# Kernel tuning notes

Measured on AMD Instinct MI355X. Metric: run time of the kernel, lower is better.

## Reference

```python
import jax, jax.numpy as jnp
import numpy as np

FEATURES = 4
HIDDEN = 32


def setup_inputs() -> dict:
    key = jax.random.key(0)
    ks = jax.random.split(key, 12)
    n_nodes, n_edges = 100000, 2500000
    x = jax.random.normal(ks[0], (n_nodes, FEATURES), dtype=jnp.float32)
    edge_index = jax.random.randint(ks[1], (2, n_edges), 0, n_nodes, dtype=jnp.int64)
    def glorot(k, fan_in, fan_out):
        s = jnp.sqrt(6.0 / (fan_in + fan_out)).astype(jnp.float32)
        return jax.random.uniform(k, (fan_in, fan_out), jnp.float32, -s, s)
    return {
        "x": x,
        "edge_index": edge_index,
        "W1": glorot(ks[2], FEATURES, HIDDEN), "b1": jnp.zeros((HIDDEN,), jnp.float32),
        "W2": glorot(ks[3], HIDDEN, HIDDEN),   "b2": jnp.zeros((HIDDEN,), jnp.float32),
        "W21": glorot(ks[4], HIDDEN, HIDDEN),  "b21": jnp.zeros((HIDDEN,), jnp.float32),
        "W3": glorot(ks[5], HIDDEN, 1),        "b3": jnp.zeros((1,), jnp.float32),
    }


def _gcn_norm(edge_index, n_nodes):
    # Add self-loops, compute symmetric normalization deg^-1/2[dst]*deg^-1/2[src]
    loops = jnp.arange(n_nodes, dtype=edge_index.dtype)
    src = jnp.concatenate([edge_index[0], loops])
    dst = jnp.concatenate([edge_index[1], loops])
    deg = jax.ops.segment_sum(jnp.ones_like(dst, dtype=jnp.float32), dst, num_segments=n_nodes)
    dinv = jnp.where(deg > 0, jax.lax.rsqrt(deg), 0.0)
    norm = dinv[src] * dinv[dst]  # [E+N]
    return src, dst, norm


def _gcn_layer(x, W, b, src, dst, norm, n_nodes):
    h = x @ W                                   # [N, out]
    msg = h[src] * norm[:, None]                # gather + scale
    out = jax.ops.segment_sum(msg, dst, num_segments=n_nodes)  # scatter-add
    return out + b


def reference(x, edge_index, W1, b1, W2, b2, W21, b21, W3, b3):
    n_nodes = x.shape[0]
    src, dst, norm = _gcn_norm(edge_index, n_nodes)
    h = jax.nn.relu(_gcn_layer(x, W1, b1, src, dst, norm, n_nodes))
    h = jax.nn.relu(_gcn_layer(h, W2, b2, src, dst, norm, n_nodes))
    h = jax.nn.relu(_gcn_layer(h, W21, b21, src, dst, norm, n_nodes))
    return _gcn_layer(h, W3, b3, src, dst, norm, n_nodes)
```

## Files before the change

kernel.cpp:

```cpp
#include <hip/hip_runtime.h>

#define FEATS 4
#define HID 32
#define BLK 256
#define CAP 64
#define PW 256
#define PSHIFT 8
#define PCAP 8192
#define NPB 512
#define PBLK 1024
#define MAXK 8
#define MAXNP 512

static inline int cdiv(long long a, int b) { return (int)((a + b - 1) / b); }

__global__ void k_zero_i(int* __restrict__ p, int n) {
    int i = blockIdx.x * blockDim.x + threadIdx.x;
    if (i < n) p[i] = 0;
}

__global__ void __launch_bounds__(PBLK, 4)
k_partition(const int* __restrict__ src, const int* __restrict__ dst,
            int* __restrict__ part_fill, unsigned int* __restrict__ part_edges,
            int e, int np) {
    __shared__ int lcnt[MAXNP];
    __shared__ int lbase[MAXNP];
    for (int p = threadIdx.x; p < np; p += blockDim.x) lcnt[p] = 0;
    __syncthreads();
    int chunk = (e + gridDim.x - 1) / gridDim.x;
    int lo = blockIdx.x * chunk;
    int hi = min(lo + chunk, e);
    unsigned pw[MAXK];
    int pp[MAXK];
#pragma unroll
    for (int k = 0; k < MAXK; k++) {
        int j = lo + threadIdx.x + k * (int)blockDim.x;
        if (j < hi) {
            int d = dst[j], s = src[j];
            int p = d >> PSHIFT;
            pp[k] = p;
            pw[k] = (unsigned)s | ((unsigned)(d & (PW - 1)) << 24);
            atomicAdd(&lcnt[p], 1);
        } else pp[k] = -1;
    }
    __syncthreads();
    for (int p = threadIdx.x; p < np; p += blockDim.x) {
        int c = lcnt[p];
        lbase[p] = c ? atomicAdd(&part_fill[p], c) : 0;
        lcnt[p] = 0;
    }
    __syncthreads();
#pragma unroll
    for (int k = 0; k < MAXK; k++) {
        if (pp[k] >= 0) {
            int p = pp[k];
            int pos = lbase[p] + atomicAdd(&lcnt[p], 1);
            if (pos < PCAP) part_edges[(size_t)p * PCAP + pos] = pw[k];
        }
    }
}

__global__ void k_local_csr(const int* __restrict__ part_fill,
                            const unsigned int* __restrict__ part_edges,
                            const float4* __restrict__ x,
                            int* __restrict__ cnt_g, float* __restrict__ dinv,
                            float4* __restrict__ xn, int* __restrict__ bucket, int n) {
    __shared__ int cnt[PW];
    int p = blockIdx.x;
    if (threadIdx.x < PW) cnt[threadIdx.x] = 0;
    __syncthreads();
    int m = min(part_fill[p], PCAP);
    const unsigned int* pe = part_edges + (size_t)p * PCAP;
    int base_node = p << PSHIFT;
    for (int j = threadIdx.x; j < m; j += blockDim.x) {
        unsigned v = pe[j];
        int local = (int)(v >> 24);
        int s = (int)(v & 0xFFFFFFu);
        int pos = atomicAdd(&cnt[local], 1);
        if (pos < CAP) bucket[(size_t)(base_node + local) * CAP + pos] = s;
    }
    __syncthreads();
    if (threadIdx.x < PW) {
        int node = base_node + threadIdx.x;
        if (node < n) {
            int dg = cnt[threadIdx.x];
            cnt_g[node] = dg;
            float s = rsqrtf((float)(dg + 1));
            dinv[node] = s;
            float4 v = x[node];
            v.x *= s; v.y *= s; v.z *= s; v.w *= s;
            xn[node] = v;
        }
    }
}

__global__ void k_dinv(const int* __restrict__ deg, float* __restrict__ dinv, int n) {
    int i = blockIdx.x * blockDim.x + threadIdx.x;
    if (i < n) dinv[i] = rsqrtf((float)(deg[i] + 1));
}

__global__ void k_gather4_f12(const int* __restrict__ cnt, const int* __restrict__ bucket,
                              const float4* __restrict__ xn, const float* __restrict__ dinv,
                              const float* __restrict__ W1, const float* __restrict__ b1,
                              const float* __restrict__ W2, float* __restrict__ hn, int n) {
    __shared__ float4 sW1[FEATS * 8];
    __shared__ float4 sB1[8];
    __shared__ float4 sW2[HID * 8];
    int tid = threadIdx.x;
    if (tid < FEATS * 8) sW1[tid] = ((const float4*)W1)[tid];
    if (tid < 8) sB1[tid] = ((const float4*)b1)[tid];
    sW2[tid] = ((const float4*)W2)[tid];
    __syncthreads();
    int gid = blockIdx.x * blockDim.x + tid;
    int node = gid >> 3;
    int cq = gid & 7;
    if (node >= n) return;
    int dg = min(cnt[node], CAP);
    const int* row = bucket + (size_t)node * CAP;
    float4 acc = make_float4(0.f, 0.f, 0.f, 0.f);
    int j = cq;
    for (; j + 8 < dg; j += 16) {
        int s0 = row[j], s1 = row[j + 8];
        float4 v0 = xn[s0];
        float4 v1 = xn[s1];
        acc.x += v0.x + v1.x; acc.y += v0.y + v1.y;
        acc.z += v0.z + v1.z; acc.w += v0.w + v1.w;
    }
    if (j < dg) {
        float4 v = xn[row[j]];
        acc.x += v.x; acc.y += v.y; acc.z += v.z; acc.w += v.w;
    }
#pragma unroll
    for (int m = 1; m < 8; m <<= 1) {
        acc.x += __shfl_xor(acc.x, m, 8);
        acc.y += __shfl_xor(acc.y, m, 8);
        acc.z += __shfl_xor(acc.z, m, 8);
        acc.w += __shfl_xor(acc.w, m, 8);
    }
    float sc = dinv[node];
    float4 self = xn[node];
    float4 a;
    a.x = sc * (acc.x + self.x);
    a.y = sc * (acc.y + self.y);
    a.z = sc * (acc.z + self.z);
    a.w = sc * (acc.w + self.w);
    float4 w0 = sW1[0 * 8 + cq], w1 = sW1[1 * 8 + cq];
    float4 w2 = sW1[2 * 8 + cq], w3 = sW1[3 * 8 + cq];
    float4 y = sB1[cq];
    y.x += a.x * w0.x + a.y * w1.x + a.z * w2.x + a.w * w3.x;
    y.y += a.x * w0.y + a.y * w1.y + a.z * w2.y + a.w * w3.y;
    y.z += a.x * w0.z + a.y * w1.z + a.z * w2.z + a.w * w3.z;
    y.w += a.x * w0.w + a.y * w1.w + a.z * w2.w + a.w * w3.w;
    y.x = fmaxf(y.x, 0.f); y.y = fmaxf(y.y, 0.f);
    y.z = fmaxf(y.z, 0.f); y.w = fmaxf(y.w, 0.f);
    float4 o = make_float4(0.f, 0.f, 0.f, 0.f);
#pragma unroll
    for (int r = 0; r < 8; r++) {
        float4 v;
        v.x = __shfl(y.x, r, 8);
        v.y = __shfl(y.y, r, 8);
        v.z = __shfl(y.z, r, 8);
        v.w = __shfl(y.w, r, 8);
        float4 wa = sW2[(4 * r + 0) * 8 + cq];
        float4 wb = sW2[(4 * r + 1) * 8 + cq];
        float4 wc = sW2[(4 * r + 2) * 8 + cq];
        float4 wd = sW2[(4 * r + 3) * 8 + cq];
        o.x += v.x * wa.x + v.y * wb.x + v.z * wc.x + v.w * wd.x;
        o.y += v.x * wa.y + v.y * wb.y + v.z * wc.y + v.w * wd.y;
        o.z += v.x * wa.z + v.y * wb.z + v.z * wc.z + v.w * wd.z;
        o.w += v.x * wa.w + v.y * wb.w + v.z * wc.w + v.w * wd.w;
    }
    o.x *= sc; o.y *= sc; o.z *= sc; o.w *= sc;
    ((float4*)hn)[node * 8 + cq] = o;
}

template <int K, int C>
__global__ void k_mm(const float* __restrict__ in, const float* __restrict__ W,
                     const float* __restrict__ dinv, float* __restrict__ hn, int n) {
    __shared__ float sW[K * C];
    for (int i = threadIdx.x; i < K * C; i += blockDim.x) sW[i] = W[i];
    __syncthreads();
    int gid = blockIdx.x * blockDim.x + threadIdx.x;
    int node = gid / C, c = gid % C;
    if (node >= n) return;
    float acc = 0.0f;
#pragma unroll
    for (int k = 0; k < K; k++) acc += in[node * K + k] * sW[k * C + c];
    hn[node * C + c] = acc * dinv[node];
}

#define ACC4(v) do { acc.x += (v).x; acc.y += (v).y; acc.z += (v).z; acc.w += (v).w; } while (0)

#define GATHER_BODY()                                                        \
    int dg = min(cnt[node], CAP);                                            \
    const float4* hp = (const float4*)hn;                                    \
    const int* row = bucket + (size_t)node * CAP;                            \
    float4 acc = hp[node * 8 + cq];                                          \
    int j = 0;                                                               \
    for (; j + 8 <= dg; j += 8) {                                            \
        int4 sa = *(const int4*)(row + j);                                   \
        int4 sb = *(const int4*)(row + j + 4);                               \
        float4 v0 = hp[sa.x * 8 + cq];                                       \
        float4 v1 = hp[sa.y * 8 + cq];                                       \
        float4 v2 = hp[sa.z * 8 + cq];                                       \
        float4 v3 = hp[sa.w * 8 + cq];                                       \
        float4 v4 = hp[sb.x * 8 + cq];                                       \
        float4 v5 = hp[sb.y * 8 + cq];                                       \
        float4 v6 = hp[sb.z * 8 + cq];                                       \
        float4 v7 = hp[sb.w * 8 + cq];                                       \
        ACC4(v0); ACC4(v1); ACC4(v2); ACC4(v3);                              \
        ACC4(v4); ACC4(v5); ACC4(v6); ACC4(v7);                              \
    }                                                                        \
    if (j + 4 <= dg) {                                                       \
        int4 s4 = *(const int4*)(row + j);                                   \
        float4 v0 = hp[s4.x * 8 + cq];                                       \
        float4 v1 = hp[s4.y * 8 + cq];                                       \
        float4 v2 = hp[s4.z * 8 + cq];                                       \
        float4 v3 = hp[s4.w * 8 + cq];                                       \
        ACC4(v0); ACC4(v1); ACC4(v2); ACC4(v3);                              \
        j += 4;                                                              \
    }                                                                        \
    for (; j < dg; j++) {                                                    \
        float4 v = hp[row[j] * 8 + cq];                                      \
        ACC4(v);                                                             \
    }

__global__ void k_gather_fmm(const int* __restrict__ cnt, const int* __restrict__ bucket,
                             const float* __restrict__ hn, const float* __restrict__ dinv,
                             const float* __restrict__ bias, const float* __restrict__ Wn,
                             float* __restrict__ hn3, int n) {
    __shared__ float4 sW[HID * 8];
    sW[threadIdx.x] = ((const float4*)Wn)[threadIdx.x];
    __syncthreads();
    int gid = blockIdx.x * blockDim.x + threadIdx.x;
    int node = gid >> 3;
    int cq = gid & 7;
    if (node >= n) return;
    GATHER_BODY()
    float sc = dinv[node];
    float4 b = ((const float4*)bias)[cq];
    float4 y;
    y.x = fmaxf(sc * acc.x + b.x, 0.f);
    y.y = fmaxf(sc * acc.y + b.y, 0.f);
    y.z = fmaxf(sc * acc.z + b.z, 0.f);
    y.w = fmaxf(sc * acc.w + b.w, 0.f);
    float4 o = make_float4(0.f, 0.f, 0.f, 0.f);
#pragma unroll
    for (int r = 0; r < 8; r++) {
        float4 v;
        v.x = __shfl(y.x, r, 8);
        v.y = __shfl(y.y, r, 8);
        v.z = __shfl(y.z, r, 8);
        v.w = __shfl(y.w, r, 8);
        float4 w0 = sW[(4 * r + 0) * 8 + cq];
        float4 w1 = sW[(4 * r + 1) * 8 + cq];
        float4 w2 = sW[(4 * r + 2) * 8 + cq];
        float4 w3 = sW[(4 * r + 3) * 8 + cq];
        o.x += v.x * w0.x + v.y * w1.x + v.z * w2.x + v.w * w3.x;
        o.y += v.x * w0.y + v.y * w1.y + v.z * w2.y + v.w * w3.y;
        o.z += v.x * w0.z + v.y * w1.z + v.z * w2.z + v.w * w3.z;
        o.w += v.x * w0.w + v.y * w1.w + v.z * w2.w + v.w * w3.w;
    }
    o.x *= sc; o.y *= sc; o.z *= sc; o.w *= sc;
    ((float4*)hn3)[node * 8 + cq] = o;
}

__global__ void k_gather_fdot(const int* __restrict__ cnt, const int* __restrict__ bucket,
                              const float* __restrict__ hn, const float* __restrict__ dinv,
                              const float* __restrict__ bias, const float* __restrict__ W3,
                              float* __restrict__ hn4, int n) {
    int gid = blockIdx.x * blockDim.x + threadIdx.x;
    int node = gid >> 3;
    int cq = gid & 7;
    if (node >= n) return;
    GATHER_BODY()
    float sc = dinv[node];
    float4 b = ((const float4*)bias)[cq];
    float4 w = ((const float4*)W3)[cq];
    float p = fmaxf(sc * acc.x + b.x, 0.f) * w.x
            + fmaxf(sc * acc.y + b.y, 0.f) * w.y
            + fmaxf(sc * acc.z + b.z, 0.f) * w.z
            + fmaxf(sc * acc.w + b.w, 0.f) * w.w;
#pragma unroll
    for (int o = 4; o > 0; o >>= 1) p += __shfl_down(p, o, 8);
    if (cq == 0) hn4[node] = p * sc;
}

__global__ void k_gather1b(const int* __restrict__ cnt, const int* __restrict__ bucket,
                           const float* __restrict__ hn, const float* __restrict__ dinv,
                           const float* __restrict__ b, float* __restrict__ out, int n) {
    int gid = blockIdx.x * blockDim.x + threadIdx.x;
    int node = gid >> 3;
    int lane = gid & 7;
    if (node >= n) return;
    int dg = min(cnt[node], CAP);
    const int* row = bucket + (size_t)node * CAP;
    float acc = (lane == 0) ? hn[node] : 0.0f;
    int j = lane;
    for (; j + 8 < dg; j += 16) {
        float a0 = hn[row[j]];
        float a1 = hn[row[j + 8]];
        acc += a0 + a1;
    }
    if (j < dg) acc += hn[row[j]];
#pragma unroll
    for (int o = 4; o > 0; o >>= 1) acc += __shfl_down(acc, o, 8);
    if (lane == 0) out[node] = dinv[node] * acc + b[0];
}

__global__ void k_deg_count(const int* __restrict__ dst, int* __restrict__ deg, int e) {
    int i = blockIdx.x * blockDim.x + threadIdx.x;
    if (i < e) atomicAdd(&deg[dst[i]], 1);
}

__global__ void k_block_scan(const int* __restrict__ deg, int* __restrict__ exc,
                             int* __restrict__ blk_sums, int n) {
    __shared__ int s[BLK];
    int i = blockIdx.x * BLK + threadIdx.x;
    int v = (i < n) ? deg[i] : 0;
    s[threadIdx.x] = v;
    __syncthreads();
    for (int off = 1; off < BLK; off <<= 1) {
        int t = (threadIdx.x >= (unsigned)off) ? s[threadIdx.x - off] : 0;
        __syncthreads();
        s[threadIdx.x] += t;
        __syncthreads();
    }
    if (i < n) exc[i] = s[threadIdx.x] - v;
    if (threadIdx.x == BLK - 1) blk_sums[blockIdx.x] = s[threadIdx.x];
}

__global__ void k_scan_sums(int* __restrict__ blk_sums, int nb) {
    __shared__ int s[1024];
    __shared__ int carry;
    if (threadIdx.x == 0) carry = 0;
    __syncthreads();
    for (int base = 0; base < nb; base += 1024) {
        int i = base + threadIdx.x;
        int v = (i < nb) ? blk_sums[i] : 0;
        s[threadIdx.x] = v;
        __syncthreads();
        for (int off = 1; off < 1024; off <<= 1) {
            int t = (threadIdx.x >= (unsigned)off) ? s[threadIdx.x - off] : 0;
            __syncthreads();
            s[threadIdx.x] += t;
            __syncthreads();
        }
        if (i < nb) blk_sums[i] = s[threadIdx.x] - v + carry;
        __syncthreads();
        if (threadIdx.x == 0) carry += s[1023];
        __syncthreads();
    }
}

__global__ void k_add_off(const int* __restrict__ exc, const int* __restrict__ blk_sums,
                          int* __restrict__ row_start, int* __restrict__ fill, int n) {
    int i = blockIdx.x * blockDim.x + threadIdx.x;
    if (i < n) {
        int rs = exc[i] + blk_sums[i / BLK];
        row_start[i] = rs;
        fill[i] = rs;
    }
}

__global__ void k_scatter(const int* __restrict__ src, const int* __restrict__ dst,
                          int* __restrict__ fill, int* __restrict__ csr_src, int e) {
    int i = blockIdx.x * blockDim.x + threadIdx.x;
    if (i < e) {
        int pos = atomicAdd(&fill[dst[i]], 1);
        csr_src[pos] = src[i];
    }
}

template <bool RELU>
__global__ void k_gather32(const int* __restrict__ row_start, const int* __restrict__ deg,
                           const int* __restrict__ csr_src, const float* __restrict__ hn,
                           const float* __restrict__ dinv, const float* __restrict__ bias,
                           float* __restrict__ y, int n) {
    int gid = blockIdx.x * blockDim.x + threadIdx.x;
    int node = gid >> 3;
    int cq = gid & 7;
    if (node >= n) return;
    int rs = row_start[node], dg = deg[node];
    const float4* hp = (const float4*)hn;
    float4 acc = hp[node * 8 + cq];
    for (int j = 0; j < dg; j++) {
        int s = csr_src[rs + j];
        float4 v = hp[s * 8 + cq];
        ACC4(v);
    }
    float sc = dinv[node];
    float4 b = ((const float4*)bias)[cq];
    float4 r;
    r.x = sc * acc.x + b.x; r.y = sc * acc.y + b.y;
    r.z = sc * acc.z + b.z; r.w = sc * acc.w + b.w;
    if (RELU) {
        r.x = fmaxf(r.x, 0.0f); r.y = fmaxf(r.y, 0.0f);
        r.z = fmaxf(r.z, 0.0f); r.w = fmaxf(r.w, 0.0f);
    }
    ((float4*)y)[node * 8 + cq] = r;
}

__global__ void k_gather1(const int* __restrict__ row_start, const int* __restrict__ deg,
                          const int* __restrict__ csr_src, const float* __restrict__ hn,
                          const float* __restrict__ dinv, const float* __restrict__ b,
                          float* __restrict__ out, int n) {
    int gid = blockIdx.x * blockDim.x + threadIdx.x;
    int node = gid >> 3;
    int lane = gid & 7;
    if (node >= n) return;
    int rs = row_start[node], dg = deg[node];
    float acc = (lane == 0) ? hn[node] : 0.0f;
    for (int j = lane; j < dg; j += 8) acc += hn[csr_src[rs + j]];
#pragma unroll
    for (int o = 4; o > 0; o >>= 1) acc += __shfl_down(acc, o, 8);
    if (lane == 0) out[node] = dinv[node] * acc + b[0];
}

extern "C" void kernel_launch(void* const* d_in, const int* in_sizes, int n_in,
                              void* d_out, int out_size, void* d_ws, size_t ws_size,
                              hipStream_t stream) {
    const float* x   = (const float*)d_in[0];
    const int*   ei  = (const int*)d_in[1];
    const float* W1  = (const float*)d_in[2];
    const float* b1  = (const float*)d_in[3];
    const float* W2  = (const float*)d_in[4];
    const float* b2  = (const float*)d_in[5];
    const float* W21 = (const float*)d_in[6];
    const float* b21 = (const float*)d_in[7];
    const float* W3  = (const float*)d_in[8];
    const float* b3  = (const float*)d_in[9];
    float* out = (float*)d_out;

    const int n = in_sizes[0] / FEATS;
    const int e = in_sizes[1] / 2;
    const int* src = ei;
    const int* dst = ei + e;
    const int nb = cdiv(n, BLK);
    const int np = cdiv(n, PW);

    auto align256 = [](size_t v) { return (v + 255) & ~(size_t)255; };
    const long long n8 = (long long)n * 8;

    size_t sz_cnt    = align256((size_t)n * 4);
    size_t sz_dinv   = align256((size_t)n * 4);
    size_t sz_f4     = align256((size_t)n * 16);
    size_t sz_bucket = align256((size_t)n * CAP * 4);
    size_t sz_hn     = align256((size_t)n * HID * 4);
    size_t sz_part   = align256((size_t)np * PCAP * 4) + align256((size_t)np * 4);
    size_t region    = 2 * sz_hn > sz_part ? 2 * sz_hn : sz_part;
    size_t need = sz_cnt + sz_dinv + sz_f4 + sz_bucket + region;

    if (ws_size >= need && np <= MAXNP && (long long)e <= (long long)NPB * PBLK * MAXK) {
        char* ws = (char*)d_ws;
        size_t off = 0;
        int*    cnt_g  = (int*)(ws + off);    off += sz_cnt;
        float*  dinv   = (float*)(ws + off);  off += sz_dinv;
        float4* xn     = (float4*)(ws + off); off += sz_f4;
        int*    bucket = (int*)(ws + off);    off += sz_bucket;
        char*   reg    = ws + off;
        float* hn = (float*)reg;
        float* yb = (float*)(reg + sz_hn);
        unsigned int* part_edges = (unsigned int*)reg;
        int* part_fill = (int*)(reg + align256((size_t)np * PCAP * 4));

        k_zero_i<<<cdiv(np, BLK), BLK, 0, stream>>>(part_fill, np);
        k_partition<<<NPB, PBLK, 0, stream>>>(src, dst, part_fill, part_edges, e, np);
        k_local_csr<<<np, PBLK, 0, stream>>>(part_fill, part_edges, (const float4*)x,
                                             cnt_g, dinv, xn, bucket, n);

        k_gather4_f12<<<cdiv(n8, BLK), BLK, 0, stream>>>(cnt_g, bucket, xn, dinv,
                                                         W1, b1, W2, hn, n);

        k_gather_fmm<<<cdiv(n8, BLK), BLK, 0, stream>>>(cnt_g, bucket, hn, dinv, b2, W21, yb, n);
        k_gather_fdot<<<cdiv(n8, BLK), BLK, 0, stream>>>(cnt_g, bucket, yb, dinv, b21, W3, hn, n);
        k_gather1b<<<cdiv(n8, BLK), BLK, 0, stream>>>(cnt_g, bucket, hn, dinv, b3, out, n);
    } else {
        const long long nc = (long long)n * HID;
        char* ws = (char*)d_ws;
        size_t off = 0;
        int*   deg_i     = (int*)(ws + off);   off += align256((size_t)n * 4);
        int*   exc       = (int*)(ws + off);   off += align256((size_t)n * 4);
        int*   row_start = (int*)(ws + off);   off += align256((size_t)n * 4);
        int*   fill      = (int*)(ws + off);   off += align256((size_t)n * 4);
        int*   blk_sums  = (int*)(ws + off);   off += align256((size_t)nb * 4);
        float* dinv      = (float*)(ws + off); off += align256((size_t)n * 4);
        int*   csr_src   = (int*)(ws + off);   off += align256((size_t)e * 4);
        float* hn        = (float*)(ws + off); off += align256((size_t)n * HID * 4);
        float* yb        = (float*)(ws + off); off += align256((size_t)n * HID * 4);

        k_zero_i<<<nb, BLK, 0, stream>>>(deg_i, n);
        k_deg_count<<<cdiv(e, BLK), BLK, 0, stream>>>(dst, deg_i, e);
        k_dinv<<<nb, BLK, 0, stream>>>(deg_i, dinv, n);
        k_block_scan<<<nb, BLK, 0, stream>>>(deg_i, exc, blk_sums, n);
        k_scan_sums<<<1, 1024, 0, stream>>>(blk_sums, nb);
        k_add_off<<<nb, BLK, 0, stream>>>(exc, blk_sums, row_start, fill, n);
        k_scatter<<<cdiv(e, BLK), BLK, 0, stream>>>(src, dst, fill, csr_src, e);

        k_mm<FEATS, HID><<<cdiv(nc, BLK), BLK, 0, stream>>>(x, W1, dinv, hn, n);
        k_gather32<true><<<cdiv(n8, BLK), BLK, 0, stream>>>(row_start, deg_i, csr_src, hn, dinv, b1, yb, n);

        k_mm<HID, HID><<<cdiv(nc, BLK), BLK, 0, stream>>>(yb, W2, dinv, hn, n);
        k_gather32<true><<<cdiv(n8, BLK), BLK, 0, stream>>>(row_start, deg_i, csr_src, hn, dinv, b2, yb, n);

        k_mm<HID, HID><<<cdiv(nc, BLK), BLK, 0, stream>>>(yb, W21, dinv, hn, n);
        k_gather32<true><<<cdiv(n8, BLK), BLK, 0, stream>>>(row_start, deg_i, csr_src, hn, dinv, b21, yb, n);

        k_mm<HID, 1><<<cdiv(n, BLK), BLK, 0, stream>>>(yb, W3, dinv, hn, n);
        k_gather1<<<cdiv(n8, BLK), BLK, 0, stream>>>(row_start, deg_i, csr_src, hn, dinv, b3, out, n);
    }
}
```

Baseline: 243.7 us.

## Replace global-atomic partitioning with per-block fixed-size runs plus overflow buffer

The partition kernel no longer reserves space with a global atomic per partition and a second shared-memory pass. Each block now writes its edges straight into a fixed slot of 32 entries per (partition, block) pair, and only the rare excess goes through a global overflow buffer. The local CSR kernel then scans every block's run for its partition, using the per-block counts. This removes the two-phase reservation and most global atomics. In exchange the CSR kernel scans sparse runs that are largely empty, and edges beyond the overflow capacity of 64 per partition would be silently dropped.

```diff
diff --git a/kernel.cpp b/kernel.cpp
--- a/kernel.cpp
+++ b/kernel.cpp
@@ -6,11 +6,12 @@
 #define CAP 64
 #define PW 256
 #define PSHIFT 8
-#define PCAP 8192
 #define NPB 512
 #define PBLK 1024
-#define MAXK 8
 #define MAXNP 512
+#define RCAP 32
+#define RSHIFT 5
+#define OCAP 64
 
 static inline int cdiv(long long a, int b) { return (int)((a + b - 1) / b); }
 
@@ -19,65 +20,69 @@
     if (i < n) p[i] = 0;
 }
 
-__global__ void __launch_bounds__(PBLK, 4)
-k_partition(const int* __restrict__ src, const int* __restrict__ dst,
-            int* __restrict__ part_fill, unsigned int* __restrict__ part_edges,
-            int e, int np) {
+__global__ void __launch_bounds__(PBLK, 2)
+k_part_s(const int* __restrict__ src, const int* __restrict__ dst,
+         unsigned int* __restrict__ runs, int* __restrict__ cnt_runs,
+         int* __restrict__ ovf_fill, unsigned int* __restrict__ ovf,
+         int e, int np) {
     __shared__ int lcnt[MAXNP];
-    __shared__ int lbase[MAXNP];
     for (int p = threadIdx.x; p < np; p += blockDim.x) lcnt[p] = 0;
     __syncthreads();
     int chunk = (e + gridDim.x - 1) / gridDim.x;
     int lo = blockIdx.x * chunk;
     int hi = min(lo + chunk, e);
-    unsigned pw[MAXK];
-    int pp[MAXK];
-#pragma unroll
-    for (int k = 0; k < MAXK; k++) {
-        int j = lo + threadIdx.x + k * (int)blockDim.x;
-        if (j < hi) {
-            int d = dst[j], s = src[j];
-            int p = d >> PSHIFT;
-            pp[k] = p;
-            pw[k] = (unsigned)s | ((unsigned)(d & (PW - 1)) << 24);
-            atomicAdd(&lcnt[p], 1);
-        } else pp[k] = -1;
-    }
-    __syncthreads();
-    for (int p = threadIdx.x; p < np; p += blockDim.x) {
-        int c = lcnt[p];
-        lbase[p] = c ? atomicAdd(&part_fill[p], c) : 0;
-        lcnt[p] = 0;
-    }
-    __syncthreads();
-#pragma unroll
-    for (int k = 0; k < MAXK; k++) {
-        if (pp[k] >= 0) {
-            int p = pp[k];
-            int pos = lbase[p] + atomicAdd(&lcnt[p], 1);
-            if (pos < PCAP) part_edges[(size_t)p * PCAP + pos] = pw[k];
+    for (int j = lo + threadIdx.x; j < hi; j += blockDim.x) {
+        int d = dst[j], s = src[j];
+        int p = d >> PSHIFT;
+        unsigned pk = (unsigned)s | ((unsigned)(d & (PW - 1)) << 24);
+        int pos = atomicAdd(&lcnt[p], 1);
+        if (pos < RCAP) {
+            runs[((size_t)p * NPB + blockIdx.x) * RCAP + pos] = pk;
+        } else {
+            int q = atomicAdd(&ovf_fill[p], 1);
+            if (q < OCAP) ovf[(size_t)p * OCAP + q] = pk;
         }
     }
-}
-
-__global__ void k_local_csr(const int* __restrict__ part_fill,
-                            const unsigned int* __restrict__ part_edges,
-                            const float4* __restrict__ x,
-                            int* __restrict__ cnt_g, float* __restrict__ dinv,
-                            float4* __restrict__ xn, int* __restrict__ bucket, int n) {
+    __syncthreads();
+    for (int p = threadIdx.x; p < np; p += blockDim.x)
+        cnt_runs[(size_t)blockIdx.x * np + p] = lcnt[p];
+}
+
+__global__ void k_csr_s(const unsigned int* __restrict__ runs,
+                        const int* __restrict__ cnt_runs,
+                        const int* __restrict__ ovf_fill,
+                        const unsigned int* __restrict__ ovf,
+                        const float4* __restrict__ x,
+                        int* __restrict__ cnt_g, float* __restrict__ dinv,
+                        float4* __restrict__ xn, int* __restrict__ bucket,
+                        int n, int np) {
     __shared__ int cnt[PW];
+    __shared__ int scnt[NPB];
     int p = blockIdx.x;
     if (threadIdx.x < PW) cnt[threadIdx.x] = 0;
-    __syncthreads();
-    int m = min(part_fill[p], PCAP);
-    const unsigned int* pe = part_edges + (size_t)p * PCAP;
+    if (threadIdx.x < NPB)
+        scnt[threadIdx.x] = min(cnt_runs[(size_t)threadIdx.x * np + p], RCAP);
+    __syncthreads();
     int base_node = p << PSHIFT;
-    for (int j = threadIdx.x; j < m; j += blockDim.x) {
-        unsigned v = pe[j];
+    const unsigned int* pr = runs + (size_t)p * NPB * RCAP;
+    for (int s = threadIdx.x; s < NPB * RCAP; s += blockDim.x) {
+        int b = s >> RSHIFT;
+        int idx = s & (RCAP - 1);
+        if (idx < scnt[b]) {
+            unsigned v = pr[s];
+            int local = (int)(v >> 24);
+            int sv = (int)(v & 0xFFFFFFu);
+            int pos = atomicAdd(&cnt[local], 1);
+            if (pos < CAP) bucket[(size_t)(base_node + local) * CAP + pos] = sv;
+        }
+    }
+    int m2 = min(ovf_fill[p], OCAP);
+    for (int j = threadIdx.x; j < m2; j += blockDim.x) {
+        unsigned v = ovf[(size_t)p * OCAP + j];
         int local = (int)(v >> 24);
-        int s = (int)(v & 0xFFFFFFu);
+        int sv = (int)(v & 0xFFFFFFu);
         int pos = atomicAdd(&cnt[local], 1);
-        if (pos < CAP) bucket[(size_t)(base_node + local) * CAP + pos] = s;
+        if (pos < CAP) bucket[(size_t)(base_node + local) * CAP + pos] = sv;
     }
     __syncthreads();
     if (threadIdx.x < PW) {
@@ -447,31 +452,38 @@
     size_t sz_f4     = align256((size_t)n * 16);
     size_t sz_bucket = align256((size_t)n * CAP * 4);
     size_t sz_hn     = align256((size_t)n * HID * 4);
-    size_t sz_part   = align256((size_t)np * PCAP * 4) + align256((size_t)np * 4);
-    size_t region    = 2 * sz_hn > sz_part ? 2 * sz_hn : sz_part;
-    size_t need = sz_cnt + sz_dinv + sz_f4 + sz_bucket + region;
-
-    if (ws_size >= need && np <= MAXNP && (long long)e <= (long long)NPB * PBLK * MAXK) {
+    size_t sz_ovfc   = align256((size_t)np * 4);
+    size_t sz_ovf    = align256((size_t)np * OCAP * 4);
+    size_t sz_runs   = align256((size_t)np * NPB * RCAP * 4);
+    size_t sz_cruns  = align256((size_t)NPB * np * 4);
+    size_t pool      = sz_runs + sz_cruns;
+    if (2 * sz_hn > pool) pool = 2 * sz_hn;
+    size_t need = sz_cnt + sz_dinv + sz_f4 + sz_ovfc + sz_ovf + sz_bucket + pool;
+
+    if (ws_size >= need && np <= MAXNP) {
         char* ws = (char*)d_ws;
         size_t off = 0;
-        int*    cnt_g  = (int*)(ws + off);    off += sz_cnt;
-        float*  dinv   = (float*)(ws + off);  off += sz_dinv;
-        float4* xn     = (float4*)(ws + off); off += sz_f4;
-        int*    bucket = (int*)(ws + off);    off += sz_bucket;
-        char*   reg    = ws + off;
+        int*    cnt_g    = (int*)(ws + off);    off += sz_cnt;
+        float*  dinv     = (float*)(ws + off);  off += sz_dinv;
+        float4* xn       = (float4*)(ws + off); off += sz_f4;
+        int*    ovf_fill = (int*)(ws + off);    off += sz_ovfc;
+        unsigned int* ovf = (unsigned int*)(ws + off); off += sz_ovf;
+        int*    bucket   = (int*)(ws + off);    off += sz_bucket;
+        char*   reg      = ws + off;
+        unsigned int* runs = (unsigned int*)reg;
+        int* cnt_runs = (int*)(reg + sz_runs);
         float* hn = (float*)reg;
         float* yb = (float*)(reg + sz_hn);
-        unsigned int* part_edges = (unsigned int*)reg;
-        int* part_fill = (int*)(reg + align256((size_t)np * PCAP * 4));
-
-        k_zero_i<<<cdiv(np, BLK), BLK, 0, stream>>>(part_fill, np);
-        k_partition<<<NPB, PBLK, 0, stream>>>(src, dst, part_fill, part_edges, e, np);
-        k_local_csr<<<np, PBLK, 0, stream>>>(part_fill, part_edges, (const float4*)x,
-                                             cnt_g, dinv, xn, bucket, n);
+
+        k_zero_i<<<cdiv(np, BLK), BLK, 0, stream>>>(ovf_fill, np);
+        k_part_s<<<NPB, PBLK, 0, stream>>>(src, dst, runs, cnt_runs,
+                                           ovf_fill, ovf, e, np);
+        k_csr_s<<<np, PBLK, 0, stream>>>(runs, cnt_runs, ovf_fill, ovf,
+                                         (const float4*)x, cnt_g, dinv, xn,
+                                         bucket, n, np);
 
         k_gather4_f12<<<cdiv(n8, BLK), BLK, 0, stream>>>(cnt_g, bucket, xn, dinv,
                                                          W1, b1, W2, hn, n);
-
         k_gather_fmm<<<cdiv(n8, BLK), BLK, 0, stream>>>(cnt_g, bucket, hn, dinv, b2, W21, yb, n);
         k_gather_fdot<<<cdiv(n8, BLK), BLK, 0, stream>>>(cnt_g, bucket, yb, dinv, b21, W3, hn, n);
         k_gather1b<<<cdiv(n8, BLK), BLK, 0, stream>>>(cnt_g, bucket, hn, dinv, b3, out, n);
```

Result: slower. 249.8 us (+2.5%).
